# Performance work log

Hardware: AMD Instinct MI355X
Metric: run time of the kernel (lower is better)

## Reference

```python
import jax, jax.numpy as jnp
import numpy as np

B, L, D = 16, 2048, 512
VOCAB = 2545
N_LAYERS, MULT = 4, 2
H = D * MULT


def _freqs_cis(dim, end, theta=10000.0):
    freqs = 1.0 / (theta ** (np.arange(0, dim, 2)[: dim // 2].astype(np.float64) / dim))
    f = np.outer(np.arange(end), freqs)
    return jnp.asarray(np.concatenate([np.cos(f), np.sin(f)], axis=-1), dtype=jnp.float32)

FREQS_CIS = _freqs_cis(D, 8192)  # [8192, D]


def setup_inputs() -> dict:
    key = jax.random.key(0)
    ks = jax.random.split(key, 16)
    tokens = jax.random.randint(ks[0], (B, L), 0, VOCAB)
    text_lens = jax.random.randint(ks[1], (B,), 256, L + 1)
    audio_lens = jax.random.randint(ks[2], (B,), 512, L + 1)
    pos = jnp.arange(L)[None, :]
    text = jnp.where(pos < text_lens[:, None], tokens, -1)          # -1 -> pad id 0 after +1
    audio_mask = pos < audio_lens[:, None]
    s = 0.02
    return {
        "text": text,
        "audio_mask": audio_mask,
        "seq_len": L,
        "embed_table": jax.random.normal(ks[3], (VOCAB + 1, D), jnp.float32) * s,
        "dw_w": jax.random.normal(ks[4], (N_LAYERS, D, 1, 7), jnp.float32) * s,
        "dw_b": jnp.zeros((N_LAYERS, D), jnp.float32),
        "ln_g": jnp.ones((N_LAYERS, D), jnp.float32),
        "ln_b": jnp.zeros((N_LAYERS, D), jnp.float32),
        "pw1_w": jax.random.normal(ks[5], (N_LAYERS, D, H), jnp.float32) * s,
        "pw1_b": jnp.zeros((N_LAYERS, H), jnp.float32),
        "grn_g": jax.random.normal(ks[6], (N_LAYERS, H), jnp.float32) * s,
        "grn_b": jax.random.normal(ks[7], (N_LAYERS, H), jnp.float32) * s,
        "pw2_w": jax.random.normal(ks[8], (N_LAYERS, H, D), jnp.float32) * s,
        "pw2_b": jnp.zeros((N_LAYERS, D), jnp.float32),
    }


def _conv_block(x, dw_w, dw_b, ln_g, ln_b, w1, b1, gg, gb, w2, b2):
    res = x
    xc = jnp.transpose(x, (0, 2, 1))  # [B, D, L]
    xc = jax.lax.conv_general_dilated(
        xc, dw_w, window_strides=(1,), padding=[(3, 3)],
        feature_group_count=xc.shape[1], dimension_numbers=("NCH", "OIH", "NCH"))
    xc = xc + dw_b[None, :, None]
    x = jnp.transpose(xc, (0, 2, 1))  # [B, L, D]
    mu = x.mean(-1, keepdims=True)
    var = ((x - mu) ** 2).mean(-1, keepdims=True)
    x = (x - mu) / jnp.sqrt(var + 1e-6) * ln_g + ln_b
    x = jax.nn.gelu(x @ w1 + b1, approximate=False)  # [B, L, H]
    # GRN: L2 norm over sequence dim
    Gx = jnp.sqrt(jnp.sum(x * x, axis=1, keepdims=True))  # [B, 1, H]
    Nx = Gx / (Gx.mean(-1, keepdims=True) + 1e-6)
    x = gg * (x * Nx) + gb + x
    x = x @ w2 + b2
    return res + x


def _average_upsample(x, text_valid_mask, audio_mask):
    # vectorized variable-length repeat-interleave (matches the torch per-sample loop)
    b, l, d = x.shape
    valid_mask = audio_mask & text_valid_mask
    audio_len = audio_mask.sum(1)            # [B]
    valid_len = valid_mask.sum(1)            # [B]
    vl = jnp.maximum(valid_len, 1)
    base = audio_len // vl
    rem = audio_len % vl
    cut = (vl - rem) * base                  # output position where repeat count bumps to base+1
    p = jnp.arange(l)[None, :]
    j = jnp.where(p < cut[:, None],
                  p // jnp.maximum(base, 1)[:, None],
                  (vl - rem)[:, None] + (p - cut[:, None]) // (base + 1)[:, None])
    j = jnp.clip(j, 0, l - 1)
    # positions of valid tokens, ascending; invalid slots pushed to the end
    pos = jnp.where(valid_mask, jnp.arange(l)[None, :], l)
    pos = jnp.sort(pos, axis=1)
    src = jnp.clip(jnp.take_along_axis(pos, j, axis=1), 0, l - 1)   # [B, L]
    out = jnp.take_along_axis(x, src[:, :, None], axis=1)
    keep = (p < audio_len[:, None]) & (valid_len[:, None] > 0)
    return jnp.where(keep[:, :, None], out, 0.0)


def reference(text, audio_mask, seq_len, embed_table, dw_w, dw_b, ln_g, ln_b,
              pw1_w, pw1_b, grn_g, grn_b, pw2_w, pw2_b):
    t = (text + 1)[:, :seq_len]              # pad id becomes 0
    text_mask = t == 0                       # [B, L] True at padding
    x = embed_table[t]                       # [B, L, D]
    x = x + FREQS_CIS[:seq_len, :]
    x = jnp.where(text_mask[:, :, None], 0.0, x)
    for i in range(dw_w.shape[0]):
        x = _conv_block(x, dw_w[i], dw_b[i], ln_g[i], ln_b[i], pw1_w[i], pw1_b[i],
                        grn_g[i], grn_b[i], pw2_w[i], pw2_b[i])
        x = jnp.where(text_mask[:, :, None], 0.0, x)
    return _average_upsample(x, ~text_mask, audio_mask)
```

## Files before the change

kernel.cpp:

```cpp
#include <hip/hip_runtime.h>
#include <hip/hip_bf16.h>

#define BB 16
#define LL 2048
#define DD 512
#define HH 1024
#define NL 4
#define MM (BB*LL)

typedef __attribute__((ext_vector_type(8))) short bh8;
typedef __attribute__((ext_vector_type(4))) float f4;
typedef __attribute__((ext_vector_type(4))) unsigned short us4;

typedef __attribute__((address_space(3))) unsigned int lds_u32;
typedef __attribute__((address_space(1))) const unsigned int glob_u32;

__device__ __forceinline__ void gld_lds16(const void* g, void* l) {
    __builtin_amdgcn_global_load_lds((glob_u32*)g, (lds_u32*)l, 16, 0, 0);
}

__device__ __forceinline__ unsigned short f2bf(float f) {
    unsigned int u = __float_as_uint(f);
    unsigned int r = (u + 0x7FFFu + ((u >> 16) & 1u)) >> 16;
    return (unsigned short)r;
}
__device__ __forceinline__ float bf2f(unsigned short u) {
    return __uint_as_float(((unsigned int)u) << 16);
}

__device__ __forceinline__ float gelu_f(float v) {
    float y = 0.7978845608028654f * v * fmaf(0.044715f, v * v, 1.0f);
    float e = __expf(2.0f * y);
    float th = 1.0f - 2.0f * __builtin_amdgcn_rcpf(e + 1.0f);
    return 0.5f * v * (1.0f + th);
}

__global__ __launch_bounds__(256) void freqs_kernel(float* __restrict__ fr) {
    int idx = blockIdx.x * 256 + threadIdx.x;
    int l = idx >> 8;
    int j = idx & 255;
    float f = exp2f(-(float)j * 0.051905126482615036f);
    float a = (float)l * f;
    fr[(size_t)l * DD + j]       = cosf(a);
    fr[(size_t)l * DD + 256 + j] = sinf(a);
}

__global__ __launch_bounds__(256) void wtrans_kernel(const float* __restrict__ w,
                                                     unsigned short* __restrict__ wt,
                                                     int R, int C) {
    __shared__ float ls[64][65];
    int layer = blockIdx.z;
    int tr = blockIdx.y;
    int tc = blockIdx.x;
    const float* src = w + (size_t)layer * R * C + (size_t)(tr * 64) * C + tc * 64;
    int t = threadIdx.x;
    #pragma unroll
    for (int s = 0; s < 4; s++) {
        int r = (t >> 4) + 16 * s, c = (t & 15) * 4;
        f4 v = *(const f4*)(src + (size_t)r * C + c);
        ls[r][c] = v.x; ls[r][c + 1] = v.y; ls[r][c + 2] = v.z; ls[r][c + 3] = v.w;
    }
    __syncthreads();
    unsigned short* dst = wt + (size_t)layer * R * C + (size_t)(tc * 64) * R + tr * 64;
    #pragma unroll
    for (int s = 0; s < 2; s++) {
        int idx = t + 256 * s;
        int c = idx >> 3;
        int r8 = (idx & 7) * 8;
        bh8 o;
        #pragma unroll
        for (int e = 0; e < 8; e++) o[e] = (short)f2bf(ls[r8 + e][c]);
        *(bh8*)(dst + (size_t)c * R + r8) = o;
    }
}

__global__ __launch_bounds__(256) void bias2_kernel(const float* __restrict__ pw2_b,
                                                    const float* __restrict__ grn_b,
                                                    const unsigned short* __restrict__ w2t,
                                                    float* __restrict__ bias2) {
    int layer = blockIdx.x;
    for (int n = threadIdx.x; n < DD; n += 256) {
        const unsigned short* wp = w2t + (size_t)layer * DD * HH + (size_t)n * HH;
        const float* gbp = grn_b + (size_t)layer * HH;
        float s = 0.f;
        for (int k8 = 0; k8 < HH; k8 += 8) {
            bh8 wv = *(const bh8*)(wp + k8);
            #pragma unroll
            for (int e = 0; e < 8; e++) s = fmaf(gbp[k8 + e], bf2f((unsigned short)wv[e]), s);
        }
        bias2[(size_t)layer * DD + n] = pw2_b[(size_t)layer * DD + n] + s;
    }
}

__global__ __launch_bounds__(64) void embed_kernel(const int* __restrict__ text,
                                                   const float* __restrict__ table,
                                                   const float* __restrict__ fr,
                                                   unsigned short* __restrict__ x) {
    int bid = blockIdx.x;
    int t = threadIdx.x;
    int l = bid & (LL - 1);
    int d0 = t * 8;
    int tok = text[bid] + 1;
    bh8 o;
    if (tok != 0) {
        const float* e = table + (size_t)tok * DD + d0;
        const float* f = fr + (size_t)l * DD + d0;
        #pragma unroll
        for (int k = 0; k < 8; k++) o[k] = (short)f2bf(e[k] + f[k]);
    } else {
        #pragma unroll
        for (int k = 0; k < 8; k++) o[k] = 0;
    }
    *(bh8*)(x + (size_t)bid * DD + d0) = o;
}

#define CCH 16
__global__ __launch_bounds__(256) void conv_ln_kernel(const unsigned short* __restrict__ x,
                                                      const float* __restrict__ dw_w,
                                                      const float* __restrict__ dw_b,
                                                      const float* __restrict__ ln_g,
                                                      const float* __restrict__ ln_b,
                                                      unsigned short* __restrict__ xln) {
    const int t = threadIdx.x;
    const int lane = t & 63, wv = t >> 6;
    const int chunk = blockIdx.x * 4 + wv;
    const int row0 = chunk * CCH;
    const int l0 = row0 & (LL - 1);
    const int d0 = lane * 8;
    const unsigned short* xb = x + ((size_t)(row0 >> 11) * LL) * DD + d0;

    float w[7][8], cb[8], g[8], be[8];
    #pragma unroll
    for (int e = 0; e < 8; e++) {
        #pragma unroll
        for (int k = 0; k < 7; k++) w[k][e] = dw_w[(d0 + e) * 7 + k];
        cb[e] = dw_b[d0 + e];
        g[e]  = ln_g[d0 + e];
        be[e] = ln_b[d0 + e];
    }

    float ring[8][8];
    #pragma unroll
    for (int ii = 0; ii < 8; ii++) {
        int i = ii - 3;
        int s = i & 7;
        int l = l0 + i;
        bool ok = (unsigned)l < LL;
        if (ok) {
            bh8 v = *(const bh8*)(xb + (size_t)l * DD);
            #pragma unroll
            for (int e = 0; e < 8; e++) ring[s][e] = bf2f((unsigned short)v[e]);
        } else {
            #pragma unroll
            for (int e = 0; e < 8; e++) ring[s][e] = 0.f;
        }
    }

    #pragma unroll
    for (int r = 0; r < CCH; r++) {
        float acc[8];
        #pragma unroll
        for (int e = 0; e < 8; e++) acc[e] = cb[e];
        #pragma unroll
        for (int k = 0; k < 7; k++) {
            int s = (r + k - 3) & 7;
            #pragma unroll
            for (int e = 0; e < 8; e++) acc[e] = fmaf(w[k][e], ring[s][e], acc[e]);
        }
        if (r + 5 <= CCH + 2) {
            int s = (r + 5) & 7;
            int l = l0 + r + 5;
            bool ok = (unsigned)l < LL;
            if (ok) {
                bh8 v = *(const bh8*)(xb + (size_t)l * DD);
                #pragma unroll
                for (int e = 0; e < 8; e++) ring[s][e] = bf2f((unsigned short)v[e]);
            } else {
                #pragma unroll
                for (int e = 0; e < 8; e++) ring[s][e] = 0.f;
            }
        }
        float s1 = 0.f, s2 = 0.f;
        #pragma unroll
        for (int e = 0; e < 8; e++) { s1 += acc[e]; s2 = fmaf(acc[e], acc[e], s2); }
        #pragma unroll
        for (int off = 1; off <= 32; off <<= 1) {
            s1 += __shfl_xor(s1, off, 64);
            s2 += __shfl_xor(s2, off, 64);
        }
        float mu = s1 * (1.0f / DD);
        float var = s2 * (1.0f / DD) - mu * mu;
        float rstd = rsqrtf(var + 1e-6f);
        bh8 o;
        #pragma unroll
        for (int e = 0; e < 8; e++) o[e] = (short)f2bf((acc[e] - mu) * rstd * g[e] + be[e]);
        *(bh8*)(xln + (size_t)(row0 + r) * DD + d0) = o;
    }
}

template<int KDIM, int NDIM, int MODE>
__global__ __launch_bounds__(512) void gemm_bf16_kernel(const unsigned short* __restrict__ A,
                                                        const unsigned short* __restrict__ Bt,
                                                        const float* __restrict__ bias,
                                                        unsigned short* __restrict__ hout,
                                                        unsigned short* __restrict__ xio,
                                                        const int* __restrict__ text,
                                                        float* __restrict__ aux) {
    __shared__ unsigned short lsbuf[65536];
    const int tid = threadIdx.x;
    constexpr int NX = NDIM / 256;
    constexpr int NWG = NX * (MM / 256);
    constexpr int NT = KDIM / 64;
    const int id = blockIdx.y * NX + blockIdx.x;
    const int sw = (id & 7) * (NWG / 8) + (id >> 3);
    const int m0 = (sw / NX) * 256;
    const int n0 = (sw % NX) * 256;

    const int lane = tid & 63, wid = tid >> 6;
    const int wm = wid >> 2, wn = wid & 3;
    const int ln = lane & 15;
    const int kq0 = ((lane >> 4) * 8) ^ ((lane & 7) << 3);
    const int kq1 = (32 + (lane >> 4) * 8) ^ ((lane & 7) << 3);
    const int arow = (wm * 128 + ln) * 64;
    const int brow = (wn * 64 + ln) * 64;

    const int srow = tid >> 3;
    const int scol = ((tid & 7) ^ (srow & 7)) << 3;
    const int sdst = tid * 8;
    const unsigned short* Asrc = A + ((size_t)m0 + srow) * KDIM + scol;
    const unsigned short* Bsrc;
    if constexpr (MODE == 0) Bsrc = Bt + ((size_t)n0 + srow) * KDIM + scol;
    else                     Bsrc = Bt + ((size_t)(m0 >> 11) * NDIM + n0 + srow) * KDIM + scol;

    f4 acc[8][4];
    #pragma unroll
    for (int i = 0; i < 8; i++)
        #pragma unroll
        for (int j = 0; j < 4; j++) acc[i][j] = (f4){0.f, 0.f, 0.f, 0.f};

#define LSA(bb) (lsbuf + (bb) * 16384)
#define LSB(bb) (lsbuf + 32768 + (bb) * 16384)
#define STG_ALL(bb, ko) do { _Pragma("unroll") for (int h = 0; h < 2; h++) {               \
    gld_lds16(Asrc + (size_t)(h * 128) * KDIM + (ko), LSA(bb) + h * 8192 + sdst);          \
    gld_lds16(Asrc + (size_t)(h * 128 + 64) * KDIM + (ko), LSA(bb) + h * 8192 + 4096 + sdst); \
    gld_lds16(Bsrc + (size_t)(h * 128) * KDIM + (ko), LSB(bb) + h * 8192 + sdst);          \
    gld_lds16(Bsrc + (size_t)(h * 128 + 64) * KDIM + (ko), LSB(bb) + h * 8192 + 4096 + sdst); } } while (0)
#define BOUNDARY do { asm volatile("s_waitcnt vmcnt(0)" ::: "memory");                     \
    __builtin_amdgcn_s_barrier(); __builtin_amdgcn_sched_barrier(0); } while (0)
#define RD_A03 do { _Pragma("unroll") for (int i = 0; i < 4; i++) {                        \
    aF[i][0] = *(bh8*)(LSA(cur) + arow + i * 1024 + kq0);                                  \
    aF[i][1] = *(bh8*)(LSA(cur) + arow + i * 1024 + kq1); } } while (0)
#define RD_A47 do { _Pragma("unroll") for (int i = 0; i < 4; i++) {                        \
    aF[i][0] = *(bh8*)(LSA(cur) + arow + (i + 4) * 1024 + kq0);                            \
    aF[i][1] = *(bh8*)(LSA(cur) + arow + (i + 4) * 1024 + kq1); } } while (0)
#define RD_B01 do { _Pragma("unroll") for (int j = 0; j < 2; j++) {                        \
    b0F[j][0] = *(bh8*)(LSB(cur) + brow + j * 1024 + kq0);                                 \
    b0F[j][1] = *(bh8*)(LSB(cur) + brow + j * 1024 + kq1); } } while (0)
#define RD_B23 do { _Pragma("unroll") for (int j = 0; j < 2; j++) {                        \
    b1F[j][0] = *(bh8*)(LSB(cur) + brow + (j + 2) * 1024 + kq0);                           \
    b1F[j][1] = *(bh8*)(LSB(cur) + brow + (j + 2) * 1024 + kq1); } } while (0)
#define MFMA_Q(i0, j0, bf) do { __builtin_amdgcn_s_setprio(1);                             \
    _Pragma("unroll") for (int i = 0; i < 4; i++)                                          \
    _Pragma("unroll") for (int j = 0; j < 2; j++) {                                        \
        acc[i + i0][j + j0] = __builtin_amdgcn_mfma_f32_16x16x32_bf16(aF[i][0], bf[j][0], acc[i + i0][j + j0], 0, 0, 0); \
        acc[i + i0][j + j0] = __builtin_amdgcn_mfma_f32_16x16x32_bf16(aF[i][1], bf[j][1], acc[i + i0][j + j0], 0, 0, 0); } \
    __builtin_amdgcn_s_setprio(0); } while (0)

    STG_ALL(0, 0);
    BOUNDARY;

    bh8 aF[4][2], b0F[2][2], b1F[2][2];
    for (int kt = 0; kt < NT; kt++) {
        const int cur = kt & 1, nb = cur ^ 1;
        const bool more = (kt + 1 < NT);
        if (more) { STG_ALL(nb, (kt + 1) * 64); }
        __builtin_amdgcn_sched_barrier(0);
        RD_A03; RD_B01;
        MFMA_Q(0, 0, b0F);
        RD_B23;
        MFMA_Q(0, 2, b1F);
        RD_A47;
        MFMA_Q(4, 2, b1F);
        MFMA_Q(4, 0, b0F);
        if (more) { BOUNDARY; }
    }
#undef STG_ALL
#undef BOUNDARY
#undef RD_A03
#undef RD_A47
#undef RD_B01
#undef RD_B23
#undef MFMA_Q
#undef LSA
#undef LSB

    const int rowOff = (lane >> 4) * 4;
    const int colOff = ln;
    if constexpr (MODE == 0) {
        float sj0[4] = {0.f, 0.f, 0.f, 0.f};
        float sj1[4] = {0.f, 0.f, 0.f, 0.f};
        #pragma unroll
        for (int i = 0; i < 8; i++) {
            #pragma unroll
            for (int j = 0; j < 4; j++) {
                int n = n0 + wn * 64 + j * 16 + colOff;
                float bn = bias[n];
                #pragma unroll
                for (int r = 0; r < 4; r++) {
                    int m = m0 + wm * 128 + i * 16 + rowOff + r;
                    float v = gelu_f(acc[i][j][r] + bn);
                    hout[(size_t)m * NDIM + n] = f2bf(v);
                    if (i < 4) sj0[j] = fmaf(v, v, sj0[j]);
                    else       sj1[j] = fmaf(v, v, sj1[j]);
                }
            }
        }
        #pragma unroll
        for (int j = 0; j < 4; j++) {
            sj0[j] += __shfl_xor(sj0[j], 16, 64);
            sj0[j] += __shfl_xor(sj0[j], 32, 64);
            sj1[j] += __shfl_xor(sj1[j], 16, 64);
            sj1[j] += __shfl_xor(sj1[j], 32, 64);
        }
        if (lane < 16) {
            int rb = (m0 + wm * 128) >> 6;
            #pragma unroll
            for (int j = 0; j < 4; j++) {
                aux[(size_t)rb * HH + n0 + wn * 64 + j * 16 + lane] = sj0[j];
                aux[(size_t)(rb + 1) * HH + n0 + wn * 64 + j * 16 + lane] = sj1[j];
            }
        }
    } else {
        __syncthreads();
        float* cf = (float*)lsbuf;
        #pragma unroll
        for (int half = 0; half < 2; half++) {
            if (wm == half) {
                #pragma unroll
                for (int i = 0; i < 8; i++)
                    #pragma unroll
                    for (int j = 0; j < 4; j++) {
                        int lc = wn * 64 + j * 16 + colOff;
                        float bn = bias[n0 + lc];
                        #pragma unroll
                        for (int r = 0; r < 4; r++) {
                            int lr = i * 16 + rowOff + r;
                            cf[lr * 256 + lc] = acc[i][j][r] + bn;
                        }
                    }
            }
            __syncthreads();
            #pragma unroll
            for (int k = 0; k < 16; k++) {
                int ci = tid + 512 * k;
                int row = ci >> 6, ch = ci & 63;
                int m = m0 + half * 128 + row;
                size_t gb = (size_t)m * NDIM + n0 + ch * 4;
                bool msk = (text[m] == -1);
                us4 xo = *(const us4*)(xio + gb);
                f4 c = *(const f4*)&cf[row * 256 + ch * 4];
                us4 onew;
                onew.x = msk ? 0 : f2bf(c.x + bf2f(xo.x));
                onew.y = msk ? 0 : f2bf(c.y + bf2f(xo.y));
                onew.z = msk ? 0 : f2bf(c.z + bf2f(xo.z));
                onew.w = msk ? 0 : f2bf(c.w + bf2f(xo.w));
                *(us4*)(xio + gb) = onew;
            }
            __syncthreads();
        }
    }
}

__global__ __launch_bounds__(256) void grn_stats_kernel(const float* __restrict__ gxp,
                                                        const float* __restrict__ gg,
                                                        float* __restrict__ scale) {
    int b = blockIdx.x, t = threadIdx.x;
    float g[4];
    float s = 0.f;
    #pragma unroll
    for (int e = 0; e < 4; e++) {
        int ch = t + e * 256;
        float acc = 0.f;
        #pragma unroll
        for (int rb = 0; rb < 32; rb++) acc += gxp[(size_t)(b * 32 + rb) * HH + ch];
        g[e] = sqrtf(acc);
        s += g[e];
    }
    #pragma unroll
    for (int off = 32; off > 0; off >>= 1) s += __shfl_down(s, off);
    __shared__ float rs[4];
    if ((t & 63) == 0) rs[t >> 6] = s;
    __syncthreads();
    float tot = rs[0] + rs[1] + rs[2] + rs[3];
    float mean = tot * (1.0f / HH);
    float inv = 1.0f / (mean + 1e-6f);
    #pragma unroll
    for (int e = 0; e < 4; e++) {
        int ch = t + e * 256;
        scale[(size_t)b * HH + ch] = fmaf(gg[ch], g[e] * inv, 1.0f);
    }
}

__global__ __launch_bounds__(256) void w2scale_kernel(const unsigned short* __restrict__ w2t,
                                                      const float* __restrict__ scale,
                                                      unsigned short* __restrict__ w2s) {
    int b = blockIdx.y;
    size_t idx = ((size_t)blockIdx.x * 256 + threadIdx.x) * 8;
    int k = (int)(idx & (HH - 1));
    bh8 w = *(const bh8*)(w2t + idx);
    f4 s0 = *(const f4*)(scale + (size_t)b * HH + k);
    f4 s1 = *(const f4*)(scale + (size_t)b * HH + k + 4);
    float sv[8] = {s0.x,s0.y,s0.z,s0.w,s1.x,s1.y,s1.z,s1.w};
    bh8 o;
    #pragma unroll
    for (int e = 0; e < 8; e++) o[e] = (short)f2bf(bf2f((unsigned short)w[e]) * sv[e]);
    *(bh8*)(w2s + (size_t)b * DD * HH + idx) = o;
}

__global__ __launch_bounds__(256) void upscan_kernel(const int* __restrict__ text,
                                                     const int* __restrict__ audio,
                                                     int* __restrict__ pos,
                                                     int* __restrict__ lens) {
    int b = blockIdx.x, t = threadIdx.x;
    int lane = t & 63, wv = t >> 6;
    __shared__ int wt[4], wa[4];
    int voff = 0, aoff = 0;
    for (int c = 0; c < LL / 256; c++) {
        int l = c * 256 + t;
        int am = audio[(size_t)b * LL + l];
        int tv = text[(size_t)b * LL + l];
        int valid = (am != 0 && tv != -1) ? 1 : 0;
        unsigned long long mv = __ballot(valid);
        unsigned long long ma = __ballot(am != 0);
        if (lane == 0) { wt[wv] = __popcll(mv); wa[wv] = __popcll(ma); }
        __syncthreads();
        int pre = 0;
        #pragma unroll
        for (int w = 0; w < 4; w++) if (w < wv) pre += wt[w];
        int incl = pre + (int)__popcll(mv << (63 - lane));
        if (valid) pos[(size_t)b * LL + voff + incl - 1] = l;
        int bt = wt[0] + wt[1] + wt[2] + wt[3];
        int ba = wa[0] + wa[1] + wa[2] + wa[3];
        __syncthreads();
        voff += bt;
        aoff += ba;
    }
    if (t == 0) { lens[b * 2] = aoff; lens[b * 2 + 1] = voff; }
    for (int i = voff + t; i < LL; i += 256) pos[(size_t)b * LL + i] = LL - 1;
}

__global__ __launch_bounds__(128) void upgather_kernel(const unsigned short* __restrict__ x,
                                                       const int* __restrict__ pos,
                                                       const int* __restrict__ lens,
                                                       float* __restrict__ out) {
    int bid = blockIdx.x;
    int b = bid >> 11;
    int p = bid & (LL - 1);
    int t = threadIdx.x;
    int alen = lens[b * 2], vlen = lens[b * 2 + 1];
    f4 v = {0.f, 0.f, 0.f, 0.f};
    if (p < alen && vlen > 0) {
        int vl = vlen < 1 ? 1 : vlen;
        int base = alen / vl, rem = alen % vl;
        int cut = (vl - rem) * base;
        int j;
        if (p < cut) j = p / (base < 1 ? 1 : base);
        else j = (vl - rem) + (p - cut) / (base + 1);
        j = j < 0 ? 0 : (j > LL - 1 ? LL - 1 : j);
        int s = pos[(size_t)b * LL + j];
        s = s < 0 ? 0 : (s > LL - 1 ? LL - 1 : s);
        us4 u = *(const us4*)(x + ((size_t)b * LL + s) * DD + t * 4);
        v.x = bf2f(u.x); v.y = bf2f(u.y); v.z = bf2f(u.z); v.w = bf2f(u.w);
    }
    *(f4*)(out + (size_t)bid * DD + t * 4) = v;
}

#define OFF_FREQS  ((size_t)0)
#define OFF_X      (OFF_FREQS + (size_t)LL * DD * 4)
#define OFF_XLN    (OFF_X + (size_t)MM * DD * 2)
#define OFF_H      (OFF_XLN + (size_t)MM * DD * 2)
#define OFF_W1T    (OFF_H + (size_t)MM * HH * 2)
#define OFF_W2T    (OFF_W1T + (size_t)NL * HH * DD * 2)
#define OFF_GXP    (OFF_W2T + (size_t)NL * DD * HH * 2)
#define OFF_NX     (OFF_GXP + (size_t)512 * HH * 4)
#define OFF_B2     (OFF_NX + (size_t)BB * HH * 4)
#define OFF_POS    (OFF_B2 + (size_t)NL * DD * 4)
#define OFF_LENS   (OFF_POS + (size_t)BB * LL * 4)
#define OFF_W2S    OFF_XLN

extern "C" void kernel_launch(void* const* d_in, const int* in_sizes, int n_in,
                              void* d_out, int out_size, void* d_ws, size_t ws_size,
                              hipStream_t stream) {
    const int*   text  = (const int*)d_in[0];
    const int*   audio = (const int*)d_in[1];
    const float* table = (const float*)d_in[3];
    const float* dw_w  = (const float*)d_in[4];
    const float* dw_b  = (const float*)d_in[5];
    const float* ln_g  = (const float*)d_in[6];
    const float* ln_b  = (const float*)d_in[7];
    const float* pw1_w = (const float*)d_in[8];
    const float* pw1_b = (const float*)d_in[9];
    const float* grn_g = (const float*)d_in[10];
    const float* grn_b = (const float*)d_in[11];
    const float* pw2_w = (const float*)d_in[12];
    const float* pw2_b = (const float*)d_in[13];
    float* out = (float*)d_out;

    char* ws = (char*)d_ws;
    float*          freqs = (float*)(ws + OFF_FREQS);
    unsigned short* x     = (unsigned short*)(ws + OFF_X);
    unsigned short* xln   = (unsigned short*)(ws + OFF_XLN);
    unsigned short* h     = (unsigned short*)(ws + OFF_H);
    unsigned short* w1t   = (unsigned short*)(ws + OFF_W1T);
    unsigned short* w2t   = (unsigned short*)(ws + OFF_W2T);
    unsigned short* w2s   = (unsigned short*)(ws + OFF_W2S);
    float*          gxp   = (float*)(ws + OFF_GXP);
    float*          nx    = (float*)(ws + OFF_NX);
    float*          bias2 = (float*)(ws + OFF_B2);
    int*            pos   = (int*)(ws + OFF_POS);
    int*            lens  = (int*)(ws + OFF_LENS);

    freqs_kernel<<<LL, 256, 0, stream>>>(freqs);
    wtrans_kernel<<<dim3(HH / 64, DD / 64, NL), 256, 0, stream>>>(pw1_w, w1t, DD, HH);
    wtrans_kernel<<<dim3(DD / 64, HH / 64, NL), 256, 0, stream>>>(pw2_w, w2t, HH, DD);
    bias2_kernel<<<NL, 256, 0, stream>>>(pw2_b, grn_b, w2t, bias2);
    embed_kernel<<<MM, 64, 0, stream>>>(text, table, freqs, x);

    for (int layer = 0; layer < NL; layer++) {
        conv_ln_kernel<<<MM / (4 * CCH), 256, 0, stream>>>(x,
            dw_w + (size_t)layer * DD * 7, dw_b + (size_t)layer * DD,
            ln_g + (size_t)layer * DD, ln_b + (size_t)layer * DD, xln);

        gemm_bf16_kernel<DD, HH, 0><<<dim3(HH / 256, MM / 256), 512, 0, stream>>>(
            xln, w1t + (size_t)layer * HH * DD, pw1_b + (size_t)layer * HH,
            h, nullptr, nullptr, gxp);

        grn_stats_kernel<<<BB, 256, 0, stream>>>(gxp, grn_g + (size_t)layer * HH, nx);

        w2scale_kernel<<<dim3(DD * HH / (256 * 8), BB), 256, 0, stream>>>(
            w2t + (size_t)layer * DD * HH, nx, w2s);

        gemm_bf16_kernel<HH, DD, 1><<<dim3(DD / 256, MM / 256), 512, 0, stream>>>(
            h, w2s, bias2 + (size_t)layer * DD,
            nullptr, x, text, gxp);
    }

    upscan_kernel<<<BB, 256, 0, stream>>>(text, audio, pos, lens);
    upgather_kernel<<<MM, 128, 0, stream>>>(x, pos, lens, out);
}
```

Measured before the change: 603.5 us.

## Halve GEMM K-tile to 32 to shrink LDS and allow two workgroups per CU

```diff
diff --git a/kernel.cpp b/kernel.cpp
--- a/kernel.cpp
+++ b/kernel.cpp
@@ -206,11 +206,11 @@
                                                         unsigned short* __restrict__ xio,
                                                         const int* __restrict__ text,
                                                         float* __restrict__ aux) {
-    __shared__ unsigned short lsbuf[65536];
+    __shared__ unsigned short lsbuf[32768];
     const int tid = threadIdx.x;
     constexpr int NX = NDIM / 256;
     constexpr int NWG = NX * (MM / 256);
-    constexpr int NT = KDIM / 64;
+    constexpr int NT = KDIM / 32;
     const int id = blockIdx.y * NX + blockIdx.x;
     const int sw = (id & 7) * (NWG / 8) + (id >> 3);
     const int m0 = (sw / NX) * 256;
@@ -219,13 +219,12 @@
     const int lane = tid & 63, wid = tid >> 6;
     const int wm = wid >> 2, wn = wid & 3;
     const int ln = lane & 15;
-    const int kq0 = ((lane >> 4) * 8) ^ ((lane & 7) << 3);
-    const int kq1 = (32 + (lane >> 4) * 8) ^ ((lane & 7) << 3);
-    const int arow = (wm * 128 + ln) * 64;
-    const int brow = (wn * 64 + ln) * 64;
-
-    const int srow = tid >> 3;
-    const int scol = ((tid & 7) ^ (srow & 7)) << 3;
+    const int kq = (((lane >> 4) ^ (ln & 3)) << 3);
+    const int arow = (wm * 128 + ln) * 32;
+    const int brow = (wn * 64 + ln) * 32;
+
+    const int srow = tid >> 2;
+    const int scol = (((tid & 3) ^ ((tid >> 2) & 3)) << 3);
     const int sdst = tid * 8;
     const unsigned short* Asrc = A + ((size_t)m0 + srow) * KDIM + scol;
     const unsigned short* Bsrc;
@@ -238,59 +237,40 @@
         #pragma unroll
         for (int j = 0; j < 4; j++) acc[i][j] = (f4){0.f, 0.f, 0.f, 0.f};
 
-#define LSA(bb) (lsbuf + (bb) * 16384)
-#define LSB(bb) (lsbuf + 32768 + (bb) * 16384)
-#define STG_ALL(bb, ko) do { _Pragma("unroll") for (int h = 0; h < 2; h++) {               \
-    gld_lds16(Asrc + (size_t)(h * 128) * KDIM + (ko), LSA(bb) + h * 8192 + sdst);          \
-    gld_lds16(Asrc + (size_t)(h * 128 + 64) * KDIM + (ko), LSA(bb) + h * 8192 + 4096 + sdst); \
-    gld_lds16(Bsrc + (size_t)(h * 128) * KDIM + (ko), LSB(bb) + h * 8192 + sdst);          \
-    gld_lds16(Bsrc + (size_t)(h * 128 + 64) * KDIM + (ko), LSB(bb) + h * 8192 + 4096 + sdst); } } while (0)
+#define LSA(bb) (lsbuf + (bb) * 8192)
+#define LSB(bb) (lsbuf + 16384 + (bb) * 8192)
+#define STG_ALL(bb, ko) do {                                                               \
+    gld_lds16(Asrc + (ko), LSA(bb) + sdst);                                                \
+    gld_lds16(Asrc + (size_t)128 * KDIM + (ko), LSA(bb) + 4096 + sdst);                    \
+    gld_lds16(Bsrc + (ko), LSB(bb) + sdst);                                                \
+    gld_lds16(Bsrc + (size_t)128 * KDIM + (ko), LSB(bb) + 4096 + sdst); } while (0)
 #define BOUNDARY do { asm volatile("s_waitcnt vmcnt(0)" ::: "memory");                     \
     __builtin_amdgcn_s_barrier(); __builtin_amdgcn_sched_barrier(0); } while (0)
-#define RD_A03 do { _Pragma("unroll") for (int i = 0; i < 4; i++) {                        \
-    aF[i][0] = *(bh8*)(LSA(cur) + arow + i * 1024 + kq0);                                  \
-    aF[i][1] = *(bh8*)(LSA(cur) + arow + i * 1024 + kq1); } } while (0)
-#define RD_A47 do { _Pragma("unroll") for (int i = 0; i < 4; i++) {                        \
-    aF[i][0] = *(bh8*)(LSA(cur) + arow + (i + 4) * 1024 + kq0);                            \
-    aF[i][1] = *(bh8*)(LSA(cur) + arow + (i + 4) * 1024 + kq1); } } while (0)
-#define RD_B01 do { _Pragma("unroll") for (int j = 0; j < 2; j++) {                        \
-    b0F[j][0] = *(bh8*)(LSB(cur) + brow + j * 1024 + kq0);                                 \
-    b0F[j][1] = *(bh8*)(LSB(cur) + brow + j * 1024 + kq1); } } while (0)
-#define RD_B23 do { _Pragma("unroll") for (int j = 0; j < 2; j++) {                        \
-    b1F[j][0] = *(bh8*)(LSB(cur) + brow + (j + 2) * 1024 + kq0);                           \
-    b1F[j][1] = *(bh8*)(LSB(cur) + brow + (j + 2) * 1024 + kq1); } } while (0)
-#define MFMA_Q(i0, j0, bf) do { __builtin_amdgcn_s_setprio(1);                             \
-    _Pragma("unroll") for (int i = 0; i < 4; i++)                                          \
-    _Pragma("unroll") for (int j = 0; j < 2; j++) {                                        \
-        acc[i + i0][j + j0] = __builtin_amdgcn_mfma_f32_16x16x32_bf16(aF[i][0], bf[j][0], acc[i + i0][j + j0], 0, 0, 0); \
-        acc[i + i0][j + j0] = __builtin_amdgcn_mfma_f32_16x16x32_bf16(aF[i][1], bf[j][1], acc[i + i0][j + j0], 0, 0, 0); } \
-    __builtin_amdgcn_s_setprio(0); } while (0)
 
     STG_ALL(0, 0);
     BOUNDARY;
 
-    bh8 aF[4][2], b0F[2][2], b1F[2][2];
     for (int kt = 0; kt < NT; kt++) {
-        const int cur = kt & 1, nb = cur ^ 1;
+        const int cur = kt & 1;
         const bool more = (kt + 1 < NT);
-        if (more) { STG_ALL(nb, (kt + 1) * 64); }
+        if (more) { STG_ALL(cur ^ 1, (kt + 1) * 32); }
         __builtin_amdgcn_sched_barrier(0);
-        RD_A03; RD_B01;
-        MFMA_Q(0, 0, b0F);
-        RD_B23;
-        MFMA_Q(0, 2, b1F);
-        RD_A47;
-        MFMA_Q(4, 2, b1F);
-        MFMA_Q(4, 0, b0F);
+        bh8 aF[8], bF[4];
+        #pragma unroll
+        for (int i = 0; i < 8; i++) aF[i] = *(bh8*)(LSA(cur) + arow + i * 512 + kq);
+        #pragma unroll
+        for (int j = 0; j < 4; j++) bF[j] = *(bh8*)(LSB(cur) + brow + j * 512 + kq);
+        __builtin_amdgcn_s_setprio(1);
+        #pragma unroll
+        for (int i = 0; i < 8; i++)
+            #pragma unroll
+            for (int j = 0; j < 4; j++)
+                acc[i][j] = __builtin_amdgcn_mfma_f32_16x16x32_bf16(aF[i], bF[j], acc[i][j], 0, 0, 0);
+        __builtin_amdgcn_s_setprio(0);
         if (more) { BOUNDARY; }
     }
 #undef STG_ALL
 #undef BOUNDARY
-#undef RD_A03
-#undef RD_A47
-#undef RD_B01
-#undef RD_B23
-#undef MFMA_Q
 #undef LSA
 #undef LSB
 
@@ -334,27 +314,30 @@
         __syncthreads();
         float* cf = (float*)lsbuf;
         #pragma unroll
-        for (int half = 0; half < 2; half++) {
+        for (int p = 0; p < 4; p++) {
+            const int half = p >> 1, qtr = p & 1;
             if (wm == half) {
                 #pragma unroll
-                for (int i = 0; i < 8; i++)
+                for (int i = 0; i < 4; i++) {
+                    int ii = qtr * 4 + i;
                     #pragma unroll
                     for (int j = 0; j < 4; j++) {
                         int lc = wn * 64 + j * 16 + colOff;
                         float bn = bias[n0 + lc];
                         #pragma unroll
                         for (int r = 0; r < 4; r++) {
-                            int lr = i * 16 + rowOff + r;
-                            cf[lr * 256 + lc] = acc[i][j][r] + bn;
+                            int lr = ii * 16 + rowOff + r - qtr * 64;
+                            cf[lr * 256 + lc] = acc[ii][j][r] + bn;
                         }
                     }
+                }
             }
             __syncthreads();
             #pragma unroll
-            for (int k = 0; k < 16; k++) {
+            for (int k = 0; k < 8; k++) {
                 int ci = tid + 512 * k;
                 int row = ci >> 6, ch = ci & 63;
-                int m = m0 + half * 128 + row;
+                int m = m0 + half * 128 + qtr * 64 + row;
                 size_t gb = (size_t)m * NDIM + n0 + ch * 4;
                 bool msk = (text[m] == -1);
                 us4 xo = *(const us4*)(xio + gb);
```

Result: slower. 655.1 us (+8.6%).
